# Kernel tuning notes

Hardware: AMD Instinct MI355X
Metric: run time of the kernel (lower is better)

Reference implementation:

```python
import jax, jax.numpy as jnp
import numpy as np

D_MODEL = 1024
HEADS = 16
D_K = D_MODEL // HEADS
D_FF = 4 * D_MODEL
EPS = 1e-6


def setup_inputs() -> dict:
    key = jax.random.key(0)
    ks = jax.random.split(key, 8)
    B, S = 2, 2048
    x = jax.random.normal(ks[0], (B, S, D_MODEL), dtype=jnp.float32)
    mask = jnp.tril(jnp.ones((S, S), dtype=jnp.float32))  # causal mask
    sd = 1.0 / np.sqrt(D_MODEL)
    Wq = jax.random.normal(ks[1], (D_MODEL, D_MODEL), dtype=jnp.float32) * sd
    Wk = jax.random.normal(ks[2], (D_MODEL, D_MODEL), dtype=jnp.float32) * sd
    Wv = jax.random.normal(ks[3], (D_MODEL, D_MODEL), dtype=jnp.float32) * sd
    Wo = jax.random.normal(ks[4], (D_MODEL, D_MODEL), dtype=jnp.float32) * sd
    W1 = jax.random.normal(ks[5], (D_FF, D_MODEL), dtype=jnp.float32) * sd  # torch Linear weight [out,in]
    W2 = jax.random.normal(ks[6], (D_MODEL, D_FF), dtype=jnp.float32) * (1.0 / np.sqrt(D_FF))
    g1 = jnp.ones((D_MODEL,), dtype=jnp.float32)
    b1 = jnp.zeros((D_MODEL,), dtype=jnp.float32)
    g2 = jnp.ones((D_MODEL,), dtype=jnp.float32)
    b2 = jnp.zeros((D_MODEL,), dtype=jnp.float32)
    return dict(x=x, mask=mask, Wq=Wq, Wk=Wk, Wv=Wv, Wo=Wo, W1=W1, W2=W2,
                g1=g1, b1=b1, g2=g2, b2=b2)


def _layernorm(x, gamma, beta):
    mean = jnp.mean(x, axis=-1, keepdims=True)
    var = jnp.var(x, axis=-1, keepdims=True, ddof=1)  # torch.var is unbiased
    return gamma * (x - mean) / jnp.sqrt(var + EPS) + beta


def reference(x, mask, Wq, Wk, Wv, Wo, W1, W2, g1, b1, g2, b2):
    B, S, D = x.shape
    def split_heads(t):
        return t.reshape(B, S, HEADS, D_K).transpose(0, 2, 1, 3)  # [B,H,S,dk]
    q = split_heads(x @ Wq.T)
    k = split_heads(x @ Wk.T)
    v = split_heads(x @ Wv.T)
    scores = jnp.einsum('bhqd,bhkd->bhqk', q, k) / np.sqrt(D_K)
    scores = jnp.where(mask == 0, -jnp.inf, scores)
    weights = jax.nn.softmax(scores, axis=-1)
    attn = jnp.einsum('bhqk,bhkd->bhqd', weights, v)
    attn = attn.transpose(0, 2, 1, 3).reshape(B, S, D) @ Wo.T
    x = _layernorm(x + attn, g1, b1)
    ff = jax.nn.relu(x @ W1.T) @ W2.T
    return _layernorm(x + ff, g2, b2)
```

## Files before the change

### kernel.cpp

```cpp
#include <hip/hip_runtime.h>

typedef __attribute__((ext_vector_type(8))) short short8;
typedef __attribute__((ext_vector_type(4))) float f32x4;
typedef unsigned short u16;

#define DEV static __device__ __forceinline__

DEV float b2f(u16 u) { union { unsigned u; float f; } c; c.u = ((unsigned)u) << 16; return c.f; }
DEV u16 f2b(float f) {
    union { float f; unsigned u; } c; c.f = f;
    unsigned u = c.u;
    u += 0x7fffu + ((u >> 16) & 1u);
    return (u16)(u >> 16);
}

DEV float wred_sum(float v) {
    #pragma unroll
    for (int o = 32; o > 0; o >>= 1) v += __shfl_xor(v, o, 64);
    return v;
}

__global__ __launch_bounds__(256) void cast_all(const float* __restrict__ x,
                                                const float* __restrict__ Wq,
                                                const float* __restrict__ Wk,
                                                const float* __restrict__ Wv,
                                                const float* __restrict__ Wo,
                                                const float* __restrict__ W1,
                                                const float* __restrict__ W2,
                                                u16* __restrict__ xb,
                                                u16* __restrict__ wqkvb,
                                                u16* __restrict__ wob,
                                                u16* __restrict__ w1b,
                                                u16* __restrict__ w2b) {
    int blk = blockIdx.x;
    const float* src; u16* dst; int boff;
    if      (blk < 2048) { src = x;  dst = xb;              boff = blk; }
    else if (blk < 2560) { src = Wq; dst = wqkvb;           boff = blk - 2048; }
    else if (blk < 3072) { src = Wk; dst = wqkvb + 1048576; boff = blk - 2560; }
    else if (blk < 3584) { src = Wv; dst = wqkvb + 2097152; boff = blk - 3072; }
    else if (blk < 4096) { src = Wo; dst = wob;             boff = blk - 3584; }
    else if (blk < 6144) { src = W1; dst = w1b;             boff = blk - 4096; }
    else                 { src = W2; dst = w2b;             boff = blk - 6144; }
    int i = boff * 2048 + threadIdx.x * 8;
    float4 a = *(const float4*)(src + i);
    float4 b = *(const float4*)(src + i + 4);
    uint4 o;
    o.x = (unsigned)f2b(a.x) | ((unsigned)f2b(a.y) << 16);
    o.y = (unsigned)f2b(a.z) | ((unsigned)f2b(a.w) << 16);
    o.z = (unsigned)f2b(b.x) | ((unsigned)f2b(b.y) << 16);
    o.w = (unsigned)f2b(b.z) | ((unsigned)f2b(b.w) << 16);
    *(uint4*)(dst + i) = o;
}

template <int OUT_MODE>
__global__ __launch_bounds__(256) void gemm128(const u16* __restrict__ A,
                                               const u16* __restrict__ Bt,
                                               void* __restrict__ Cout,
                                               int M, int N, int Kd,
                                               int GMx, int GNx, int cxs) {
    __shared__ __attribute__((aligned(16))) u16 As[2][4096];
    __shared__ __attribute__((aligned(16))) u16 Bs[2][4096];

    const int tid  = threadIdx.x;
    const int wid  = tid >> 6;
    const int lane = tid & 63;
    const int quad = lane >> 4;
    const int l16  = lane & 15;
    const int wm   = wid & 1;
    const int wn   = wid >> 1;

    const int id  = blockIdx.x;
    const int xcd = id & 7;
    const int s   = id >> 3;
    const int xr  = xcd >> cxs;
    const int xc  = xcd & ((1 << cxs) - 1);
    const int nl  = s % GNx;
    const int ml  = s / GNx;
    const int m0  = (xr * GMx + ml) * 128;
    const int n0  = (xc * GNx + nl) * 128;

    const int c0 = tid, c1 = 256 + tid;
    const int mA0 = c0 >> 2, mA1 = c1 >> 2;
    const int kg0 = (c0 & 3) ^ ((mA0 ^ (mA0 >> 2)) & 3);
    const int kg1 = (c1 & 3) ^ ((mA1 ^ (mA1 >> 2)) & 3);
    const u16* ga0 = A  + (size_t)(m0 + mA0) * Kd + kg0 * 8;
    const u16* ga1 = A  + (size_t)(m0 + mA1) * Kd + kg1 * 8;
    const u16* gb0 = Bt + (size_t)(n0 + mA0) * Kd + kg0 * 8;
    const u16* gb1 = Bt + (size_t)(n0 + mA1) * Kd + kg1 * 8;
    u16* const lA0 = &As[0][c0 * 8]; u16* const lA1 = &As[0][c1 * 8];
    u16* const lB0 = &Bs[0][c0 * 8]; u16* const lB1 = &Bs[0][c1 * 8];
    u16* const hA0 = &As[1][c0 * 8]; u16* const hA1 = &As[1][c1 * 8];
    u16* const hB0 = &Bs[1][c0 * 8]; u16* const hB1 = &Bs[1][c1 * 8];

    f32x4 acc[4][4] = {};

    int mfr[4], nfr[4];
    #pragma unroll
    for (int t = 0; t < 4; ++t) {
        int m = wm * 64 + t * 16 + l16;
        mfr[t] = m * 32 + (quad ^ ((m ^ (m >> 2)) & 3)) * 8;
        int n = wn * 64 + t * 16 + l16;
        nfr[t] = n * 32 + (quad ^ ((n ^ (n >> 2)) & 3)) * 8;
    }

    #define COMPUTE(buf)                                                      \
        do {                                                                  \
            short8 af[4], bf[4];                                              \
            _Pragma("unroll")                                                 \
            for (int t = 0; t < 4; ++t) af[t] = *(const short8*)&As[buf][mfr[t]]; \
            _Pragma("unroll")                                                 \
            for (int t = 0; t < 4; ++t) bf[t] = *(const short8*)&Bs[buf][nfr[t]]; \
            _Pragma("unroll")                                                 \
            for (int mt = 0; mt < 4; ++mt)                                    \
                _Pragma("unroll")                                             \
                for (int nt = 0; nt < 4; ++nt)                                \
                    acc[mt][nt] = __builtin_amdgcn_mfma_f32_16x16x32_bf16(af[mt], bf[nt], acc[mt][nt], 0, 0, 0); \
        } while (0)

    const int NT = Kd >> 5;
    uint4 e0, e1, e2, e3;
    uint4 o0, o1, o2, o3;

    e0 = *(const uint4*)(ga0); e1 = *(const uint4*)(ga1);
    e2 = *(const uint4*)(gb0); e3 = *(const uint4*)(gb1);
    *(uint4*)lA0 = e0; *(uint4*)lA1 = e1;
    *(uint4*)lB0 = e2; *(uint4*)lB1 = e3;
    e0 = *(const uint4*)(ga0 + 32); e1 = *(const uint4*)(ga1 + 32);
    e2 = *(const uint4*)(gb0 + 32); e3 = *(const uint4*)(gb1 + 32);
    __syncthreads();

    for (int t = 0; t < NT; t += 2) {
        if (t + 2 < NT) {
            int kk = (t + 2) * 32;
            o0 = *(const uint4*)(ga0 + kk); o1 = *(const uint4*)(ga1 + kk);
            o2 = *(const uint4*)(gb0 + kk); o3 = *(const uint4*)(gb1 + kk);
        }
        *(uint4*)hA0 = e0; *(uint4*)hA1 = e1;
        *(uint4*)hB0 = e2; *(uint4*)hB1 = e3;
        COMPUTE(0);
        __syncthreads();
        if (t + 3 < NT) {
            int kk = (t + 3) * 32;
            e0 = *(const uint4*)(ga0 + kk); e1 = *(const uint4*)(ga1 + kk);
            e2 = *(const uint4*)(gb0 + kk); e3 = *(const uint4*)(gb1 + kk);
        }
        if (t + 2 < NT) {
            *(uint4*)lA0 = o0; *(uint4*)lA1 = o1;
            *(uint4*)lB0 = o2; *(uint4*)lB1 = o3;
        }
        COMPUTE(1);
        __syncthreads();
    }
    #undef COMPUTE

    #pragma unroll
    for (int mt = 0; mt < 4; ++mt) {
        #pragma unroll
        for (int nt = 0; nt < 4; ++nt) {
            #pragma unroll
            for (int r = 0; r < 4; ++r) {
                int row = m0 + wm * 64 + mt * 16 + quad * 4 + r;
                int col = n0 + wn * 64 + nt * 16 + l16;
                float v = acc[mt][nt][r];
                if (OUT_MODE == 1) v = fmaxf(v, 0.f);
                if (OUT_MODE == 2) {
                    ((float*)Cout)[(size_t)row * N + col] = v;
                } else {
                    ((u16*)Cout)[(size_t)row * N + col] = f2b(v);
                }
            }
        }
    }
}

#define QS 3072
__global__ __launch_bounds__(256) void attn_mfma(const u16* __restrict__ QKV,
                                                 u16* __restrict__ Om) {
    __shared__ __attribute__((aligned(16))) u16 K_sh[64][72];
    __shared__ __attribute__((aligned(16))) u16 V_sh[64][72];
    __shared__ __attribute__((aligned(16))) u16 P_sh[4][32][72];

    const int tid  = threadIdx.x;
    const int wid  = tid >> 6;
    const int lane = tid & 63;
    const int quad = lane >> 4;
    const int l16  = lane & 15;
    const int bh   = blockIdx.x & 31;
    const int b    = bh >> 4, h = bh & 15;
    const int qt   = 15 - (blockIdx.x >> 5);
    const int S = 2048, Dm = 1024;
    const int q0w = qt * 128 + wid * 32;

    const u16* Qm = QKV;
    const u16* Km = QKV + 1024;
    const u16* Vm = QKV + 2048;

    short8 bq[2][2];
    #pragma unroll
    for (int qs = 0; qs < 2; ++qs)
        #pragma unroll
        for (int dc = 0; dc < 2; ++dc)
            bq[qs][dc] = *(const short8*)(Qm + (size_t)(b * S + q0w + qs * 16 + l16) * QS
                                             + h * 64 + dc * 32 + quad * 8);

    float mS[2] = { -INFINITY, -INFINITY };
    float lS[2] = { 0.f, 0.f };
    f32x4 accO[4][2] = {};

    const int ntiles = qt * 2 + 2;
    for (int t = 0; t < ntiles; ++t) {
        const int k0 = t * 64;
        __syncthreads();
        #pragma unroll
        for (int it = 0; it < 2; ++it) {
            int key = (tid >> 3) + it * 32;
            int dcol = (tid & 7) * 8;
            *(uint4*)&K_sh[key][dcol] =
                *(const uint4*)(Km + (size_t)(b * S + k0 + key) * QS + h * 64 + dcol);
        }
        #pragma unroll
        for (int it = 0; it < 2; ++it) {
            int key = lane;
            int d0 = wid * 8 + it * 32;
            uint4 vv = *(const uint4*)(Vm + (size_t)(b * S + k0 + key) * QS + h * 64 + d0);
            const u16* ve = (const u16*)&vv;
            #pragma unroll
            for (int j = 0; j < 8; ++j) V_sh[d0 + j][key] = ve[j];
        }
        __syncthreads();

        if (k0 > q0w + 31) continue;

        f32x4 sC[4][2] = {};
        #pragma unroll
        for (int dc = 0; dc < 2; ++dc)
            #pragma unroll
            for (int st = 0; st < 4; ++st) {
                short8 ak = *(const short8*)&K_sh[st * 16 + l16][dc * 32 + quad * 8];
                #pragma unroll
                for (int qs = 0; qs < 2; ++qs)
                    sC[st][qs] = __builtin_amdgcn_mfma_f32_16x16x32_bf16(ak, bq[qs][dc], sC[st][qs], 0, 0, 0);
            }

        if (k0 + 63 > q0w) {
            #pragma unroll
            for (int st = 0; st < 4; ++st)
                #pragma unroll
                for (int qs = 0; qs < 2; ++qs)
                    #pragma unroll
                    for (int r = 0; r < 4; ++r) {
                        int key = k0 + st * 16 + quad * 4 + r;
                        int qq  = q0w + qs * 16 + l16;
                        sC[st][qs][r] = (key > qq) ? -INFINITY : sC[st][qs][r] * 0.125f;
                    }
        } else {
            #pragma unroll
            for (int st = 0; st < 4; ++st)
                #pragma unroll
                for (int qs = 0; qs < 2; ++qs)
                    #pragma unroll
                    for (int r = 0; r < 4; ++r) sC[st][qs][r] *= 0.125f;
        }

        #pragma unroll
        for (int qs = 0; qs < 2; ++qs) {
            float tmax = -INFINITY;
            #pragma unroll
            for (int st = 0; st < 4; ++st)
                #pragma unroll
                for (int r = 0; r < 4; ++r) tmax = fmaxf(tmax, sC[st][qs][r]);
            tmax = fmaxf(tmax, __shfl_xor(tmax, 16, 64));
            tmax = fmaxf(tmax, __shfl_xor(tmax, 32, 64));
            float mnew = fmaxf(mS[qs], tmax);
            float al = __expf(mS[qs] - mnew);
            mS[qs] = mnew;
            float rs = 0.f;
            #pragma unroll
            for (int st = 0; st < 4; ++st) {
                u16 pk[4];
                #pragma unroll
                for (int r = 0; r < 4; ++r) {
                    float p = __expf(sC[st][qs][r] - mnew);
                    rs += p;
                    pk[r] = f2b(p);
                }
                *(ushort4*)&P_sh[wid][qs * 16 + l16][st * 16 + quad * 4] =
                    make_ushort4(pk[0], pk[1], pk[2], pk[3]);
            }
            rs += __shfl_xor(rs, 16, 64);
            rs += __shfl_xor(rs, 32, 64);
            lS[qs] = lS[qs] * al + rs;
            #pragma unroll
            for (int dm = 0; dm < 4; ++dm)
                #pragma unroll
                for (int r = 0; r < 4; ++r) accO[dm][qs][r] *= al;
        }

        #pragma unroll
        for (int kc = 0; kc < 2; ++kc) {
            short8 bp[2];
            #pragma unroll
            for (int qs = 0; qs < 2; ++qs)
                bp[qs] = *(const short8*)&P_sh[wid][qs * 16 + l16][kc * 32 + quad * 8];
            #pragma unroll
            for (int dm = 0; dm < 4; ++dm) {
                short8 av = *(const short8*)&V_sh[dm * 16 + l16][kc * 32 + quad * 8];
                #pragma unroll
                for (int qs = 0; qs < 2; ++qs)
                    accO[dm][qs] = __builtin_amdgcn_mfma_f32_16x16x32_bf16(av, bp[qs], accO[dm][qs], 0, 0, 0);
            }
        }
    }

    __syncthreads();

    #pragma unroll
    for (int qs = 0; qs < 2; ++qs) {
        float rl = 1.f / lS[qs];
        #pragma unroll
        for (int dm = 0; dm < 4; ++dm) {
            u16 pk[4];
            #pragma unroll
            for (int r = 0; r < 4; ++r) pk[r] = f2b(accO[dm][qs][r] * rl);
            *(ushort4*)&P_sh[wid][qs * 16 + l16][dm * 16 + quad * 4] =
                make_ushort4(pk[0], pk[1], pk[2], pk[3]);
        }
    }
    __syncthreads();
    #pragma unroll
    for (int pass = 0; pass < 4; ++pass) {
        int qq = pass * 8 + (lane >> 3);
        int dd = (lane & 7) * 8;
        uint4 v = *(const uint4*)&P_sh[wid][qq][dd];
        *(uint4*)(Om + (size_t)(b * S + q0w + qq) * Dm + h * 64 + dd) = v;
    }
}

__global__ __launch_bounds__(256) void ln1_kernel(const float* __restrict__ xin,
                                                  const float* __restrict__ addf,
                                                  const float* __restrict__ g,
                                                  const float* __restrict__ bb,
                                                  float* __restrict__ x1f,
                                                  u16* __restrict__ x1b) {
    __shared__ float red[8];
    const int row = blockIdx.x, tid = threadIdx.x;
    const int wid = tid >> 6, lane = tid & 63;
    const float* xr = xin + (size_t)row * 1024;
    const float* ar = addf + (size_t)row * 1024;

    float v[4], s = 0.f, sq = 0.f;
    #pragma unroll
    for (int j = 0; j < 4; ++j) {
        int i = tid + 256 * j;
        float t = xr[i] + ar[i];
        v[j] = t; s += t; sq += t * t;
    }
    s = wred_sum(s); sq = wred_sum(sq);
    if (lane == 0) { red[wid] = s; red[4 + wid] = sq; }
    __syncthreads();
    s  = red[0] + red[1] + red[2] + red[3];
    sq = red[4] + red[5] + red[6] + red[7];

    float mean = s * (1.f / 1024.f);
    float var  = (sq - s * mean) * (1.f / 1023.f);
    float rstd = rsqrtf(var + 1e-6f);

    #pragma unroll
    for (int j = 0; j < 4; ++j) {
        int i = tid + 256 * j;
        float o = g[i] * ((v[j] - mean) * rstd) + bb[i];
        x1f[(size_t)row * 1024 + i] = o;
        x1b[(size_t)row * 1024 + i] = f2b(o);
    }
}

__global__ __launch_bounds__(256) void ln2_kernel(const float* __restrict__ x1f,
                                                  const float* __restrict__ addf,
                                                  const float* __restrict__ g,
                                                  const float* __restrict__ bb,
                                                  float* __restrict__ out) {
    __shared__ float red[8];
    const int row = blockIdx.x, tid = threadIdx.x;
    const int wid = tid >> 6, lane = tid & 63;
    const float* xr = x1f + (size_t)row * 1024;
    const float* ar = addf + (size_t)row * 1024;

    float v[4], s = 0.f, sq = 0.f;
    #pragma unroll
    for (int j = 0; j < 4; ++j) {
        int i = tid + 256 * j;
        float t = xr[i] + ar[i];
        v[j] = t; s += t; sq += t * t;
    }
    s = wred_sum(s); sq = wred_sum(sq);
    if (lane == 0) { red[wid] = s; red[4 + wid] = sq; }
    __syncthreads();
    s  = red[0] + red[1] + red[2] + red[3];
    sq = red[4] + red[5] + red[6] + red[7];

    float mean = s * (1.f / 1024.f);
    float var  = (sq - s * mean) * (1.f / 1023.f);
    float rstd = rsqrtf(var + 1e-6f);

    #pragma unroll
    for (int j = 0; j < 4; ++j) {
        int i = tid + 256 * j;
        out[(size_t)row * 1024 + i] = g[i] * ((v[j] - mean) * rstd) + bb[i];
    }
}

extern "C" void kernel_launch(void* const* d_in, const int* in_sizes, int n_in,
                              void* d_out, int out_size, void* d_ws, size_t ws_size,
                              hipStream_t stream) {
    (void)in_sizes; (void)n_in; (void)out_size; (void)ws_size;
    const float* x  = (const float*)d_in[0];
    const float* Wq = (const float*)d_in[2];
    const float* Wk = (const float*)d_in[3];
    const float* Wv = (const float*)d_in[4];
    const float* Wo = (const float*)d_in[5];
    const float* W1 = (const float*)d_in[6];
    const float* W2 = (const float*)d_in[7];
    const float* g1 = (const float*)d_in[8];
    const float* b1 = (const float*)d_in[9];
    const float* g2 = (const float*)d_in[10];
    const float* b2 = (const float*)d_in[11];
    float* out = (float*)d_out;

    char* w = (char*)d_ws;
    const size_t MB = 1024ull * 1024ull;
    u16*   xb    = (u16*)(w + 0 * MB);
    u16*   Wqkvb = (u16*)(w + 8 * MB);
    u16*   Wob   = (u16*)(w + 14 * MB);
    u16*   W1b   = (u16*)(w + 16 * MB);
    u16*   W2b   = (u16*)(w + 24 * MB);
    u16*   QKVb  = (u16*)(w + 32 * MB);
    u16*   ffb   = (u16*)(w + 32 * MB);
    u16*   attnb = (u16*)(w + 64 * MB);
    u16*   x1b   = (u16*)(w + 72 * MB);
    float* tmpf  = (float*)(w + 80 * MB);
    float* x1f   = (float*)(w + 96 * MB);

    dim3 blk(256);
    cast_all<<<8192, blk, 0, stream>>>(x, Wq, Wk, Wv, Wo, W1, W2,
                                       xb, Wqkvb, Wob, W1b, W2b);

    gemm128<0><<<768, blk, 0, stream>>>(xb, Wqkvb, QKVb, 4096, 3072, 1024, 16, 6, 2);

    attn_mfma<<<512, blk, 0, stream>>>(QKVb, attnb);

    gemm128<2><<<256, blk, 0, stream>>>(attnb, Wob, tmpf, 4096, 1024, 1024, 8, 4, 1);
    ln1_kernel<<<4096, blk, 0, stream>>>(x, tmpf, g1, b1, x1f, x1b);

    gemm128<1><<<1024, blk, 0, stream>>>(x1b, W1b, ffb, 4096, 4096, 1024, 16, 8, 2);
    gemm128<2><<<256, blk, 0, stream>>>(ffb, W2b, tmpf, 4096, 1024, 4096, 8, 4, 1);
    ln2_kernel<<<4096, blk, 0, stream>>>(x1f, tmpf, g2, b2, out);
}
```

Measured before the change: 398.6 us.

## Split-K the Wo and W2 GEMMs with bf16 partials summed in LayerNorm

Splits the K dimension of the Wo projection into 2 chunks and the W2 projection into 4 chunks, so those N=1024 GEMMs launch 512 and 1024 workgroups instead of 256 and fill more CUs. Each chunk writes its partial result as bf16 into a separate buffer, and the LayerNorm kernels add up the partials while doing the residual sum, so no extra reduction kernel is needed. The cost is that the partials are rounded to bf16 before summing, which loses accuracy. It also means more partial traffic and that workspace regions get reused.

```diff
diff --git a/kernel.cpp b/kernel.cpp
--- a/kernel.cpp
+++ b/kernel.cpp
@@ -56,8 +56,10 @@
 __global__ __launch_bounds__(256) void gemm128(const u16* __restrict__ A,
                                                const u16* __restrict__ Bt,
                                                void* __restrict__ Cout,
-                                               int M, int N, int Kd,
-                                               int GMx, int GNx, int cxs) {
+                                               u16* __restrict__ C2,
+                                               int M, int N, int Kc, int ldK,
+                                               int GMx, int GNx, int cxs,
+                                               int cshift) {
     __shared__ __attribute__((aligned(16))) u16 As[2][4096];
     __shared__ __attribute__((aligned(16))) u16 Bs[2][4096];
 
@@ -69,7 +71,8 @@
     const int wm   = wid & 1;
     const int wn   = wid >> 1;
 
-    const int id  = blockIdx.x;
+    const int cid = blockIdx.x >> cshift;
+    const int id  = blockIdx.x & ((1u << cshift) - 1);
     const int xcd = id & 7;
     const int s   = id >> 3;
     const int xr  = xcd >> cxs;
@@ -78,15 +81,16 @@
     const int ml  = s / GNx;
     const int m0  = (xr * GMx + ml) * 128;
     const int n0  = (xc * GNx + nl) * 128;
+    const int kbase = cid * Kc;
 
     const int c0 = tid, c1 = 256 + tid;
     const int mA0 = c0 >> 2, mA1 = c1 >> 2;
     const int kg0 = (c0 & 3) ^ ((mA0 ^ (mA0 >> 2)) & 3);
     const int kg1 = (c1 & 3) ^ ((mA1 ^ (mA1 >> 2)) & 3);
-    const u16* ga0 = A  + (size_t)(m0 + mA0) * Kd + kg0 * 8;
-    const u16* ga1 = A  + (size_t)(m0 + mA1) * Kd + kg1 * 8;
-    const u16* gb0 = Bt + (size_t)(n0 + mA0) * Kd + kg0 * 8;
-    const u16* gb1 = Bt + (size_t)(n0 + mA1) * Kd + kg1 * 8;
+    const u16* ga0 = A  + (size_t)(m0 + mA0) * ldK + kbase + kg0 * 8;
+    const u16* ga1 = A  + (size_t)(m0 + mA1) * ldK + kbase + kg1 * 8;
+    const u16* gb0 = Bt + (size_t)(n0 + mA0) * ldK + kbase + kg0 * 8;
+    const u16* gb1 = Bt + (size_t)(n0 + mA1) * ldK + kbase + kg1 * 8;
     u16* const lA0 = &As[0][c0 * 8]; u16* const lA1 = &As[0][c1 * 8];
     u16* const lB0 = &Bs[0][c0 * 8]; u16* const lB1 = &Bs[0][c1 * 8];
     u16* const hA0 = &As[1][c0 * 8]; u16* const hA1 = &As[1][c1 * 8];
@@ -117,7 +121,7 @@
                     acc[mt][nt] = __builtin_amdgcn_mfma_f32_16x16x32_bf16(af[mt], bf[nt], acc[mt][nt], 0, 0, 0); \
         } while (0)
 
-    const int NT = Kd >> 5;
+    const int NT = Kc >> 5;
     uint4 e0, e1, e2, e3;
     uint4 o0, o1, o2, o3;
 
@@ -153,6 +157,12 @@
     }
     #undef COMPUTE
 
+    u16* ob;
+    if (OUT_MODE != 2) {
+        ob = (cid < 2) ? (u16*)Cout : C2;
+        ob += (size_t)(cid & 1) * ((size_t)M * N);
+    }
+
     #pragma unroll
     for (int mt = 0; mt < 4; ++mt) {
         #pragma unroll
@@ -166,7 +176,7 @@
                 if (OUT_MODE == 2) {
                     ((float*)Cout)[(size_t)row * N + col] = v;
                 } else {
-                    ((u16*)Cout)[(size_t)row * N + col] = f2b(v);
+                    ob[(size_t)row * N + col] = f2b(v);
                 }
             }
         }
@@ -336,8 +346,9 @@
     }
 }
 
+#define PMN 4194304ull
 __global__ __launch_bounds__(256) void ln1_kernel(const float* __restrict__ xin,
-                                                  const float* __restrict__ addf,
+                                                  const u16* __restrict__ wp,
                                                   const float* __restrict__ g,
                                                   const float* __restrict__ bb,
                                                   float* __restrict__ x1f,
@@ -346,13 +357,13 @@
     const int row = blockIdx.x, tid = threadIdx.x;
     const int wid = tid >> 6, lane = tid & 63;
     const float* xr = xin + (size_t)row * 1024;
-    const float* ar = addf + (size_t)row * 1024;
+    const u16* pr = wp + (size_t)row * 1024;
 
     float v[4], s = 0.f, sq = 0.f;
     #pragma unroll
     for (int j = 0; j < 4; ++j) {
         int i = tid + 256 * j;
-        float t = xr[i] + ar[i];
+        float t = xr[i] + b2f(pr[i]) + b2f(pr[i + PMN]);
         v[j] = t; s += t; sq += t * t;
     }
     s = wred_sum(s); sq = wred_sum(sq);
@@ -375,7 +386,8 @@
 }
 
 __global__ __launch_bounds__(256) void ln2_kernel(const float* __restrict__ x1f,
-                                                  const float* __restrict__ addf,
+                                                  const u16* __restrict__ plo,
+                                                  const u16* __restrict__ phi,
                                                   const float* __restrict__ g,
                                                   const float* __restrict__ bb,
                                                   float* __restrict__ out) {
@@ -383,13 +395,15 @@
     const int row = blockIdx.x, tid = threadIdx.x;
     const int wid = tid >> 6, lane = tid & 63;
     const float* xr = x1f + (size_t)row * 1024;
-    const float* ar = addf + (size_t)row * 1024;
+    const u16* pl = plo + (size_t)row * 1024;
+    const u16* ph = phi + (size_t)row * 1024;
 
     float v[4], s = 0.f, sq = 0.f;
     #pragma unroll
     for (int j = 0; j < 4; ++j) {
         int i = tid + 256 * j;
-        float t = xr[i] + ar[i];
+        float t = xr[i] + b2f(pl[i]) + b2f(pl[i + PMN])
+                        + b2f(ph[i]) + b2f(ph[i + PMN]);
         v[j] = t; s += t; sq += t * t;
     }
     s = wred_sum(s); sq = wred_sum(sq);
@@ -435,23 +449,30 @@
     u16*   W2b   = (u16*)(w + 24 * MB);
     u16*   QKVb  = (u16*)(w + 32 * MB);
     u16*   ffb   = (u16*)(w + 32 * MB);
+    u16*   woP   = (u16*)(w + 32 * MB);
     u16*   attnb = (u16*)(w + 64 * MB);
     u16*   x1b   = (u16*)(w + 72 * MB);
-    float* tmpf  = (float*)(w + 80 * MB);
+    u16*   w2Plo = (u16*)(w + 0 * MB);
+    u16*   w2Phi = (u16*)(w + 64 * MB);
     float* x1f   = (float*)(w + 96 * MB);
 
     dim3 blk(256);
     cast_all<<<8192, blk, 0, stream>>>(x, Wq, Wk, Wv, Wo, W1, W2,
                                        xb, Wqkvb, Wob, W1b, W2b);
 
-    gemm128<0><<<768, blk, 0, stream>>>(xb, Wqkvb, QKVb, 4096, 3072, 1024, 16, 6, 2);
+    gemm128<0><<<768, blk, 0, stream>>>(xb, Wqkvb, QKVb, nullptr,
+                                        4096, 3072, 1024, 1024, 16, 6, 2, 30);
 
     attn_mfma<<<512, blk, 0, stream>>>(QKVb, attnb);
 
-    gemm128<2><<<256, blk, 0, stream>>>(attnb, Wob, tmpf, 4096, 1024, 1024, 8, 4, 1);
-    ln1_kernel<<<4096, blk, 0, stream>>>(x, tmpf, g1, b1, x1f, x1b);
-
-    gemm128<1><<<1024, blk, 0, stream>>>(x1b, W1b, ffb, 4096, 4096, 1024, 16, 8, 2);
-    gemm128<2><<<256, blk, 0, stream>>>(ffb, W2b, tmpf, 4096, 1024, 4096, 8, 4, 1);
-    ln2_kernel<<<4096, blk, 0, stream>>>(x1f, tmpf, g2, b2, out);
-}
+    gemm128<0><<<512, blk, 0, stream>>>(attnb, Wob, woP, nullptr,
+                                        4096, 1024, 512, 1024, 8, 4, 1, 8);
+    ln1_kernel<<<4096, blk, 0, stream>>>(x, woP, g1, b1, x1f, x1b);
+
+    gemm128<1><<<1024, blk, 0, stream>>>(x1b, W1b, ffb, nullptr,
+                                         4096, 4096, 1024, 1024, 16, 8, 2, 30);
+
+    gemm128<0><<<1024, blk, 0, stream>>>(ffb, W2b, w2Plo, w2Phi,
+                                         4096, 1024, 1024, 4096, 8, 4, 1, 8);
+    ln2_kernel<<<4096, blk, 0, stream>>>(x1f, w2Plo, w2Phi, g2, b2, out);
+}
```

After: 361.8 us. 1.1x faster.
